# Optimization experiments

Hardware: AMD Instinct MI355X
Metric: run time of the kernel (lower is better)

## Reference

```python
import jax, jax.numpy as jnp
from jax import lax
import numpy as np

HID = 150     # FFNN hidden dim
EMB = 300     # GloVe dim (input_dim)
LSTM = 200    # lstm_dim -> state_dim = 400
T = 768       # tokens in doc
VOCAB = 50000


def _ffnn(x, W1, b1, W2, b2, W3, b3):
    h = jax.nn.relu(x @ W1.T + b1)
    h = jax.nn.relu(h @ W2.T + b2)
    return h @ W3.T + b3


def _lstm_dir(x, Wih, Whh, b):
    H = Whh.shape[1]
    def step(carry, xt):
        h, c = carry
        z = xt @ Wih.T + h @ Whh.T + b
        i, f, g, o = jnp.split(z, 4, axis=-1)
        c = jax.nn.sigmoid(f) * c + jax.nn.sigmoid(i) * jnp.tanh(g)
        h = jax.nn.sigmoid(o) * jnp.tanh(c)
        return (h, c), h
    init = (jnp.zeros((H,), x.dtype), jnp.zeros((H,), x.dtype))
    _, hs = lax.scan(step, init, x)
    return hs


def setup_inputs():
    key = jax.random.key(0)
    ks = iter(jax.random.split(key, 40))
    def w(shape, s=0.05):
        return jax.random.normal(next(ks), shape, jnp.float32) * s
    state = 2 * LSTM
    span = 2 * state + EMB + 1   # 1101
    pair = 3 * span              # 3303
    z = lambda n: jnp.zeros((n,), jnp.float32)
    return {
        'tokens': jax.random.randint(next(ks), (T,), 0, VOCAB),
        'emb': w((VOCAB, EMB), 0.3),
        'Wih_f': w((4 * LSTM, EMB)), 'Whh_f': w((4 * LSTM, LSTM)), 'b_f': z(4 * LSTM),
        'Wih_b': w((4 * LSTM, EMB)), 'Whh_b': w((4 * LSTM, LSTM)), 'b_b': z(4 * LSTM),
        'aW1': w((HID, state)), 'ab1': z(HID), 'aW2': w((HID, HID)), 'ab2': z(HID), 'aW3': w((1, HID)), 'ab3': z(1),
        'sW1': w((HID, span)), 'sb1': z(HID), 'sW2': w((HID, HID)), 'sb2': z(HID), 'sW3': w((1, HID)), 'sb3': z(1),
        'pW1': w((HID, pair)), 'pb1': z(HID), 'pW2': w((HID, HID)), 'pb2': z(HID), 'pW3': w((1, HID)), 'pb3': z(1),
    }


def reference(tokens, emb, Wih_f, Whh_f, b_f, Wih_b, Whh_b, b_b,
              aW1, ab1, aW2, ab2, aW3, ab3,
              sW1, sb1, sW2, sb2, sW3, sb3,
              pW1, pb1, pW2, pb2, pW3, pb3):
    Tn = tokens.shape[0]
    x = emb[tokens]  # (T, 300) frozen GloVe embeds
    h = jnp.concatenate([_lstm_dir(x, Wih_f, Whh_f, b_f),
                         _lstm_dir(x[::-1], Wih_b, Whh_b, b_b)[::-1]], axis=-1)  # (T, 400)
    # dropout omitted (eval mode / identity)
    attn_logits = _ffnn(h, aW1, ab1, aW2, ab2, aW3, ab3)[:, 0]  # per-token attn score (T,)
    gs, i1s, i2s = [], [], []
    for n in range(1, 11):  # span widths 1..10
        starts = jnp.arange(Tn - n + 1)
        idx = starts[:, None] + jnp.arange(n)[None, :]           # (S_n, n)
        wgt = jax.nn.softmax(attn_logits[idx], axis=-1)          # per-span softmax over LSTM-state scores
        pooled = jnp.einsum('sn,snd->sd', wgt, x[idx])           # attention pools raw embeds (as original)
        g = jnp.concatenate([h[starts], h[starts + n - 1], pooled,
                             jnp.full((Tn - n + 1, 1), float(n), jnp.float32)], axis=-1)
        gs.append(g); i1s.append(starts); i2s.append(starts + n - 1)
    g = jnp.concatenate(gs, 0)                                    # (S, 1101)
    i1 = jnp.concatenate(i1s, 0); i2 = jnp.concatenate(i2s, 0)
    S = g.shape[0]
    sm = _ffnn(g, sW1, sb1, sW2, sb2, sW3, sb3)[:, 0]             # span scores (S,)
    order = jnp.argsort(-sm)                                      # stable desc sort, as Python sorted(reverse=True)
    i1o, i2o = i1[order], i2[order]
    # greedy overlap filter: keep span if fully taken OR both endpoints free; mark taken only when kept
    def body(k, carry):
        taken, keep = carry
        a, b = i1o[k], i2o[k]
        offs = jnp.clip(a + jnp.arange(10), 0, Tn - 1)
        valid = (a + jnp.arange(10)) <= b
        all_taken = jnp.all(jnp.where(valid, taken[offs], True))
        ok = all_taken | (~taken[a] & ~taken[b])
        keep = keep.at[k].set(ok)
        taken = taken.at[offs].max(valid & ok)
        return (taken, keep)
    _, keep = lax.fori_loop(0, S, body, (jnp.zeros((Tn,), bool), jnp.zeros((S,), bool)))
    K = int(round(Tn * 0.4))
    rank = jnp.cumsum(keep.astype(jnp.int32))
    pos = jnp.where(keep & (rank <= K), rank - 1, S)
    sel = jnp.argsort(pos)[:K]            # first K kept spans, score order (>=T width-1 spans always kept)
    sel = sel[jnp.argsort(i1o[sel])]      # stable sort by span start
    g_f = g[order][sel]; sm_f = sm[order][sel]
    i1_f = i1o[sel]; i2_f = i2o[sel]
    ii, jj = np.tril_indices(K, -1)       # row-major == nested (i, j<i) loop order
    pairs = jnp.concatenate([g_f[ii], g_f[jj], g_f[ii] * g_f[jj]], axis=-1)  # (P, 3303)
    sa = _ffnn(pairs, pW1, pb1, pW2, pb2, pW3, pb3)[:, 0]
    # sij[i, j] = sm_i + sm_j + sa_ij for j < i; diag/upper = 0 (the epsilon antecedent)
    sij = jnp.zeros((K, K), jnp.float32).at[ii, jj].set(sm_f[ii] + sm_f[jj] + sa)
    return sij, i1_f, i2_f
```

## Files before the change

### kernel.cpp

```cpp
#include <hip/hip_runtime.h>
#include <math.h>
#include <float.h>

#define TN      768
#define EMBD    300
#define XPAD    304
#define LSTMD   200
#define G4      800
#define STATE   400
#define HIDD    150
#define NPADC   160
#define SPAND   1101
#define KP      1120
#define NSPANS  7635
#define NSEL    307
#define SORTN   8192

typedef unsigned long long ull;

#define OFF_X       0u
#define OFF_ZXF     233472u
#define OFF_ZXB     847872u
#define OFF_H       1462272u
#define OFF_ATTN    1769472u
#define OFF_I1      1770496u
#define OFF_I2      1778176u
#define OFF_SM      1785856u
#define OFF_SELK    1793536u
#define OFF_SELSPAN 1794048u
#define OFF_SMF     1794560u
#define OFF_A       1795072u
#define OFF_B       1844224u
#define OFF_WTF     1893376u
#define OFF_WTB     2133376u
#define OFF_AW1T    2373376u
#define OFF_AW2T    2437376u
#define OFF_SW1T    2461376u
#define OFF_SW2T    2640576u
#define OFF_PW1AT   2664576u
#define OFF_PW1BT   2843776u
#define OFF_PW1CT   3022976u
#define OFF_PW2T    3202176u
#define OFF_G       3226176u

#define REP50(M) M(0) M(1) M(2) M(3) M(4) M(5) M(6) M(7) M(8) M(9) \
 M(10) M(11) M(12) M(13) M(14) M(15) M(16) M(17) M(18) M(19) \
 M(20) M(21) M(22) M(23) M(24) M(25) M(26) M(27) M(28) M(29) \
 M(30) M(31) M(32) M(33) M(34) M(35) M(36) M(37) M(38) M(39) \
 M(40) M(41) M(42) M(43) M(44) M(45) M(46) M(47) M(48) M(49)

__device__ __forceinline__ float sigf(float x) { return 1.f / (1.f + __expf(-x)); }
__device__ __forceinline__ float tanhf_(float x) {
    x = fminf(15.f, fmaxf(-15.f, x));
    float e = __expf(2.f * x);
    return (e - 1.f) / (e + 1.f);
}

__global__ void k_gather(const int* __restrict__ tokens, const float* __restrict__ emb,
                         float* __restrict__ x) {
    int t = blockIdx.x;
    int tok = tokens[t];
    for (int d = threadIdx.x; d < XPAD; d += 256)
        x[t * XPAD + d] = (d < EMBD) ? emb[(size_t)tok * EMBD + d] : 0.f;
}

__global__ void k_transpose(const float* __restrict__ src, float* __restrict__ dst,
                            int N, int K, int srcStride, int colOff, int Npad) {
    int k = blockIdx.x;
    int n = blockIdx.y * 256 + threadIdx.x;
    if (n >= Npad) return;
    float v = 0.f;
    if (k < K && n < N) v = src[(size_t)n * srcStride + colOff + k];
    dst[(size_t)k * Npad + n] = v;
}

__global__ void k_zx(const float* __restrict__ x, const float* __restrict__ WTf,
                     const float* __restrict__ WTb, const float* __restrict__ bf,
                     const float* __restrict__ bb, float* __restrict__ zxf,
                     float* __restrict__ zxb) {
    __shared__ float xl[8 * XPAD];
    int tid = threadIdx.x;
    int bm = blockIdx.x, dir = blockIdx.y;
    for (int l = tid; l < 8 * XPAD; l += 256) xl[l] = x[(size_t)(bm * 8) * XPAD + l];
    __syncthreads();
    const float* WT = dir ? WTb : WTf;
    const float* bv = dir ? bb : bf;
    float* zx = dir ? zxb : zxf;
    for (int jj = 0; jj < 4; ++jj) {
        int n = tid + 256 * jj;
        if (n >= G4) break;
        float acc[8] = {0, 0, 0, 0, 0, 0, 0, 0};
        for (int k = 0; k < EMBD; ++k) {
            float wv = WT[(size_t)k * G4 + n];
#pragma unroll
            for (int r = 0; r < 8; ++r) acc[r] = fmaf(xl[r * XPAD + k], wv, acc[r]);
        }
        float bias = bv[n];
#pragma unroll
        for (int r = 0; r < 8; ++r) {
            int row = bm * 8 + r;
            int trow = dir ? (TN - 1 - row) : row;
            zx[(size_t)trow * G4 + n] = acc[r] + bias;
        }
    }
}

__global__ __launch_bounds__(256, 1) void k_lstm_mb8(const float* __restrict__ zxf,
                                                     const float* __restrict__ zxb,
                                                     const float* __restrict__ Whh_f,
                                                     const float* __restrict__ Whh_b,
                                                     float* __restrict__ hcat,
                                                     ull* __restrict__ hqL2,
                                                     ull* __restrict__ hqL3) {
    int blk = blockIdx.x;
    int lane8 = blk & 7;
    if (lane8 >= 2) return;
    int dir = lane8, b = blk >> 3;
    int tid = threadIdx.x;

    const float* zx = dir ? zxb : zxf;
    const float* Whh = dir ? Whh_b : Whh_f;
    ull* hq2d = hqL2 + (size_t)dir * TN * 256;
    ull* hq3d = hqL3 + (size_t)dir * TN * 256;
    __shared__ __align__(16) float hprev[LSTMD];
    __shared__ float zl[200];
    bool active = tid < 200;
    int q = tid / 50, u = tid % 50;
    int gr_row = q * 200 + b * 50 + u;
    int grs = active ? gr_row : 0;
    const float4* wr = (const float4*)(Whh + (size_t)grs * LSTMD);
#define WDECL(i) float4 w##i = wr[i];
    REP50(WDECL)
#undef WDECL
    float c = 0.f;
    for (int l = tid; l < LSTMD; l += 256) hprev[l] = 0.f;
    int remote_idx = (tid < b * 50) ? tid : tid + 50;
    int use_fast = 4;
    __syncthreads();
    float zpre = zx[grs];
    for (int t = 0; t < TN; ++t) {
        float acc = zpre;
        const float4* h4 = (const float4*)hprev;
#define WFMA(i) { float4 hv = h4[i]; \
        acc = fmaf(w##i.x, hv.x, acc); acc = fmaf(w##i.y, hv.y, acc); \
        acc = fmaf(w##i.z, hv.z, acc); acc = fmaf(w##i.w, hv.w, acc); }
        REP50(WFMA)
#undef WFMA
        if (active) zl[tid] = acc;
        __syncthreads();
        int trow = dir ? (TN - 1 - t) : t;
        if (tid < 50) {
            float zi = zl[tid], zf = zl[50 + tid], zg = zl[100 + tid], zo = zl[150 + tid];
            c = sigf(zf) * c + sigf(zi) * tanhf_(zg);
            float h = sigf(zo) * tanhf_(c);
            hcat[(size_t)trow * STATE + dir * LSTMD + b * 50 + tid] = h;
            hprev[b * 50 + tid] = h;
            if (t + 1 < TN) {
                ull pk = (ull)__float_as_uint(h) | ((ull)(unsigned)(t + 1) << 32);
                size_t slot = (size_t)t * 256 + b * 50 + tid;
                (void)__hip_atomic_exchange(&hq2d[slot], pk, __ATOMIC_RELAXED,
                                            __HIP_MEMORY_SCOPE_WORKGROUP);
                __hip_atomic_store(&hq3d[slot], pk, __ATOMIC_RELAXED,
                                   __HIP_MEMORY_SCOPE_AGENT);
            }
        }
        if (t + 1 < TN) {
            zpre = zx[(size_t)(t + 1) * G4 + grs];
            if (tid < 150) {
                size_t slot = (size_t)t * 256 + remote_idx;
                ull v = 0;
                bool got = false;
                if (use_fast > 0) {
                    for (int it = 0; it < 8; ++it) {
                        ull probe = ~0ull;
                        __hip_atomic_compare_exchange_strong(
                            &hq2d[slot], &probe, ~0ull, __ATOMIC_RELAXED,
                            __ATOMIC_RELAXED, __HIP_MEMORY_SCOPE_WORKGROUP);
                        if ((unsigned)(probe >> 32) == (unsigned)(t + 1)) {
                            v = probe; got = true; break;
                        }
                    }
                    use_fast = got ? 4 : (use_fast - 1);
                }
                if (!got) {
                    do {
                        v = __hip_atomic_load(&hq3d[slot], __ATOMIC_RELAXED,
                                              __HIP_MEMORY_SCOPE_AGENT);
                    } while ((unsigned)(v >> 32) != (unsigned)(t + 1));
                }
                hprev[remote_idx] = __uint_as_float((unsigned)v);
            }
            __syncthreads();
        }
    }
}

__global__ void k_attn(const float* __restrict__ hcat, const float* __restrict__ aW1T,
                       const float* __restrict__ ab1, const float* __restrict__ aW2T,
                       const float* __restrict__ ab2, const float* __restrict__ aW3,
                       const float* __restrict__ ab3, float* __restrict__ attn) {
    __shared__ float hrow[STATE];
    __shared__ float l1[NPADC];
    __shared__ float l2[NPADC];
    __shared__ float red[256];
    int t = blockIdx.x, tid = threadIdx.x;
    for (int d = tid; d < STATE; d += 256) hrow[d] = hcat[(size_t)t * STATE + d];
    __syncthreads();
    if (tid < HIDD) {
        float acc = ab1[tid];
        for (int k = 0; k < STATE; ++k) acc = fmaf(hrow[k], aW1T[(size_t)k * NPADC + tid], acc);
        l1[tid] = fmaxf(acc, 0.f);
    }
    __syncthreads();
    if (tid < HIDD) {
        float acc = ab2[tid];
        for (int k = 0; k < HIDD; ++k) acc = fmaf(l1[k], aW2T[(size_t)k * NPADC + tid], acc);
        l2[tid] = fmaxf(acc, 0.f);
    }
    __syncthreads();
    float partial = (tid < HIDD) ? l2[tid] * aW3[tid] : 0.f;
    red[tid] = partial;
    __syncthreads();
    for (int s = 128; s > 0; s >>= 1) {
        if (tid < s) red[tid] += red[tid + s];
        __syncthreads();
    }
    if (tid == 0) attn[t] = red[0] + ab3[0];
}

__global__ void k_spans(const float* __restrict__ attn, const float* __restrict__ hcat,
                        const float* __restrict__ x, float* __restrict__ g,
                        int* __restrict__ i1s, int* __restrict__ i2s) {
    int s = blockIdx.x;
    int n = 1, base = 0;
    while (s >= base + (TN - n + 1)) { base += TN - n + 1; n++; }
    int a = s - base, b = a + n - 1;
    int lane = threadIdx.x;
    float e[10];
    float mx = -FLT_MAX;
#pragma unroll
    for (int k = 0; k < 10; ++k)
        if (k < n) { e[k] = attn[a + k]; mx = fmaxf(mx, e[k]); }
    float ssum = 0.f;
#pragma unroll
    for (int k = 0; k < 10; ++k)
        if (k < n) { e[k] = __expf(e[k] - mx); ssum += e[k]; }
    float w[10];
#pragma unroll
    for (int k = 0; k < 10; ++k) w[k] = (k < n) ? e[k] / ssum : 0.f;

    float* grow = g + (size_t)s * KP;
    for (int d = lane; d < STATE; d += 64) grow[d] = hcat[(size_t)a * STATE + d];
    for (int d = lane; d < STATE; d += 64) grow[STATE + d] = hcat[(size_t)b * STATE + d];
    for (int d = lane; d < EMBD; d += 64) {
        float p = 0.f;
#pragma unroll
        for (int k = 0; k < 10; ++k)
            if (k < n) p = fmaf(w[k], x[(size_t)(a + k) * XPAD + d], p);
        grow[2 * STATE + d] = p;
    }
    if (lane == 0) { grow[1100] = (float)n; i1s[s] = a; i2s[s] = b; }
    for (int d = SPAND + lane; d < KP; d += 64) grow[d] = 0.f;
}

__global__ void k_sm(const float* __restrict__ g, const float* __restrict__ sW1T,
                     const float* __restrict__ sb1, const float* __restrict__ sW2T,
                     const float* __restrict__ sb2, const float* __restrict__ sW3,
                     const float* __restrict__ sb3, float* __restrict__ smo) {
    __shared__ float As[32 * 33];
    __shared__ float Bs[32 * NPADC];
    __shared__ float L1[32 * 161];
    int tid = threadIdx.x;
    int tx = tid & 31, ty = tid >> 5;
    int row0 = blockIdx.x * 32;
    float acc[4][5] = {};
    for (int kb = 0; kb < KP; kb += 32) {
        for (int l = tid; l < 32 * 32; l += 256) {
            int r = l >> 5, cc = l & 31;
            int gr = row0 + r;
            As[r * 33 + cc] = (gr < NSPANS) ? g[(size_t)gr * KP + kb + cc] : 0.f;
        }
        for (int l = tid; l < 32 * NPADC; l += 256) {
            int r = l / NPADC, cc = l - NPADC * r;
            Bs[l] = sW1T[(size_t)(kb + r) * NPADC + cc];
        }
        __syncthreads();
        for (int kk = 0; kk < 32; ++kk) {
            float bv[5];
#pragma unroll
            for (int jn = 0; jn < 5; ++jn) bv[jn] = Bs[kk * NPADC + tx + 32 * jn];
#pragma unroll
            for (int i4 = 0; i4 < 4; ++i4) {
                float av = As[(ty * 4 + i4) * 33 + kk];
#pragma unroll
                for (int jn = 0; jn < 5; ++jn) acc[i4][jn] = fmaf(av, bv[jn], acc[i4][jn]);
            }
        }
        __syncthreads();
    }
#pragma unroll
    for (int i4 = 0; i4 < 4; ++i4)
#pragma unroll
        for (int jn = 0; jn < 5; ++jn) {
            int nn = tx + 32 * jn;
            float v = acc[i4][jn] + (nn < HIDD ? sb1[nn] : 0.f);
            L1[(ty * 4 + i4) * 161 + nn] = fmaxf(v, 0.f);
        }
    __syncthreads();
    float acc2[4][5] = {};
    for (int kk = 0; kk < HIDD; ++kk) {
        float bv[5];
#pragma unroll
        for (int jn = 0; jn < 5; ++jn) bv[jn] = sW2T[(size_t)kk * NPADC + tx + 32 * jn];
#pragma unroll
        for (int i4 = 0; i4 < 4; ++i4) {
            float av = L1[(ty * 4 + i4) * 161 + kk];
#pragma unroll
            for (int jn = 0; jn < 5; ++jn) acc2[i4][jn] = fmaf(av, bv[jn], acc2[i4][jn]);
        }
    }
    float part[4];
#pragma unroll
    for (int i4 = 0; i4 < 4; ++i4) {
        float p = 0.f;
#pragma unroll
        for (int jn = 0; jn < 5; ++jn) {
            int nn = tx + 32 * jn;
            float v = acc2[i4][jn] + (nn < HIDD ? sb2[nn] : 0.f);
            v = fmaxf(v, 0.f);
            p = fmaf(v, (nn < HIDD ? sW3[nn] : 0.f), p);
        }
        part[i4] = p;
    }
    for (int s = 16; s > 0; s >>= 1)
#pragma unroll
        for (int i4 = 0; i4 < 4; ++i4) part[i4] += __shfl_xor(part[i4], s, 32);
    if (tx == 0)
#pragma unroll
        for (int i4 = 0; i4 < 4; ++i4) {
            int gr = row0 + ty * 4 + i4;
            if (gr < NSPANS) smo[gr] = part[i4] + sb3[0];
        }
}

__global__ __launch_bounds__(1024) void k_sortsel(const float* __restrict__ sm,
                                                  const int* __restrict__ i1s,
                                                  const int* __restrict__ i2s,
                                                  int* __restrict__ selk,
                                                  int* __restrict__ selspan,
                                                  float* __restrict__ smf,
                                                  float* __restrict__ out) {
    __shared__ float ks[SORTN];
    __shared__ unsigned short id16[SORTN];
    __shared__ int ka2[512];
    __shared__ int va2[512];
    int tid = threadIdx.x;
    for (int i = tid; i < SORTN; i += 1024) {
        ks[i] = (i < NSPANS) ? sm[i] : -FLT_MAX;
        id16[i] = (unsigned short)i;
    }
    __syncthreads();
    for (int size = 2; size <= SORTN; size <<= 1) {
        for (int stride = size >> 1; stride > 0; stride >>= 1) {
            for (int t = tid; t < SORTN / 2; t += 1024) {
                int i = ((t & ~(stride - 1)) << 1) | (t & (stride - 1));
                int j = i + stride;
                float ki = ks[i], kj = ks[j];
                unsigned short ai = id16[i], aj = id16[j];
                bool less_ji = (kj > ki) || (kj == ki && aj < ai);
                bool asc = ((i & size) == 0);
                if (less_ji == asc) {
                    ks[i] = kj; ks[j] = ki;
                    id16[i] = aj; id16[j] = ai;
                }
            }
            __syncthreads();
        }
    }
    unsigned* abu = reinterpret_cast<unsigned*>(ks);
    for (int k = tid; k < NSPANS; k += 1024) {
        int sid = id16[k];
        abu[k] = (unsigned)i1s[sid] | ((unsigned)i2s[sid] << 16);
    }
    __syncthreads();
    if (tid < 64) {
        int l = tid;
        unsigned tk = 0;
        int cnt = 0;
        for (int k = 0; k < NSPANS && cnt < NSEL; ++k) {
            unsigned ab = abu[k];
            int a = (int)(ab & 0xFFFFu), b = (int)(ab >> 16);
            int lo = a - (l << 5), hi = b - (l << 5);
            lo = lo < 0 ? 0 : lo;
            hi = hi > 31 ? 31 : hi;
            unsigned m = 0;
            if (hi >= lo) {
                unsigned upper = (hi == 31) ? 0xFFFFFFFFu : ((1u << (hi + 1)) - 1u);
                m = upper & ~((1u << lo) - 1u);
            }
            bool cov = ((tk & m) == m);
            bool all_taken = __all((int)cov);
            int la = a >> 5, lb = b >> 5;
            unsigned long long bal_a = __ballot((int)((l == la) && ((tk >> (a & 31)) & 1u)));
            unsigned long long bal_b = __ballot((int)((l == lb) && ((tk >> (b & 31)) & 1u)));
            bool ok = all_taken || (bal_a == 0ull && bal_b == 0ull);
            if (ok) {
                tk |= m;
                if (l == 0) selk[cnt] = k;
                cnt++;
            }
        }
    }
    __syncthreads();
    if (tid < 512) {
        int r = tid;
        int key = 0x7FFFFFFF;
        if (r < NSEL) {
            int k = selk[r];
            int a = (int)(abu[k] & 0xFFFFu);
            key = (a << 9) | r;
        }
        ka2[r] = key;
        va2[r] = r;
    }
    __syncthreads();
    for (int size = 2; size <= 512; size <<= 1) {
        for (int stride = size >> 1; stride > 0; stride >>= 1) {
            if (tid < 256) {
                int t = tid;
                int i = ((t & ~(stride - 1)) << 1) | (t & (stride - 1));
                int j = i + stride;
                int ki = ka2[i], kj = ka2[j];
                bool asc = ((i & size) == 0);
                if ((kj < ki) == asc) {
                    ka2[i] = kj; ka2[j] = ki;
                    int vi = va2[i]; va2[i] = va2[j]; va2[j] = vi;
                }
            }
            __syncthreads();
        }
    }
    if (tid < NSEL) {
        int r = va2[tid];
        int k = selk[r];
        int sid = id16[k];
        unsigned ab = abu[k];
        selspan[tid] = sid;
        smf[tid] = sm[sid];
        out[NSEL * NSEL + tid] = (float)(ab & 0xFFFFu);
        out[NSEL * NSEL + NSEL + tid] = (float)(ab >> 16);
    }
}

__global__ void k_AB(const float* __restrict__ g, const int* __restrict__ selspan,
                     const float* __restrict__ pW1aT, const float* __restrict__ pW1bT,
                     const float* __restrict__ pb1, float* __restrict__ Aw,
                     float* __restrict__ Bw) {
    __shared__ float grow[KP];
    int r = blockIdx.x, which = blockIdx.y;
    int sid = selspan[r];
    int tid = threadIdx.x;
    for (int d = tid; d < KP; d += 256) grow[d] = g[(size_t)sid * KP + d];
    __syncthreads();
    if (tid < NPADC) {
        const float* WT = which ? pW1bT : pW1aT;
        float acc = 0.f;
        for (int k = 0; k < KP; ++k) acc = fmaf(grow[k], WT[(size_t)k * NPADC + tid], acc);
        if (which == 0) acc += (tid < HIDD ? pb1[tid] : 0.f);
        (which ? Bw : Aw)[(size_t)r * NPADC + tid] = acc;
    }
}

__global__ void k_pairs(const float* __restrict__ g, const int* __restrict__ selspan,
                        const float* __restrict__ smf, const float* __restrict__ Aw,
                        const float* __restrict__ Bw, const float* __restrict__ pW1cT,
                        const float* __restrict__ pW2T, const float* __restrict__ pb2,
                        const float* __restrict__ pW3, const float* __restrict__ pb3,
                        float* __restrict__ out) {
    int i = blockIdx.x;
    int j0 = blockIdx.y * 32;
    if (j0 >= i) return;
    __shared__ float Gj[32 * 33];
    __shared__ float Gi[32];
    __shared__ float Bs[32 * NPADC];
    __shared__ float L1s[32 * 161];
    int tid = threadIdx.x;
    int tx = tid & 31, ty = tid >> 5;
    int sidi = selspan[i];
    float acc[4][5] = {};
    for (int kb = 0; kb < KP; kb += 32) {
        for (int l = tid; l < 32 * 32; l += 256) {
            int r = l >> 5, cc = l & 31;
            int j = j0 + r;
            int sidj = selspan[j < i ? j : 0];
            Gj[r * 33 + cc] = (j < i) ? g[(size_t)sidj * KP + kb + cc] : 0.f;
        }
        if (tid < 32) Gi[tid] = g[(size_t)sidi * KP + kb + tid];
        for (int l = tid; l < 32 * NPADC; l += 256) {
            int r = l / NPADC, cc = l - NPADC * r;
            Bs[l] = pW1cT[(size_t)(kb + r) * NPADC + cc];
        }
        __syncthreads();
        for (int kk = 0; kk < 32; ++kk) {
            float gik = Gi[kk];
            float bv[5];
#pragma unroll
            for (int jn = 0; jn < 5; ++jn) bv[jn] = Bs[kk * NPADC + tx + 32 * jn];
#pragma unroll
            for (int i4 = 0; i4 < 4; ++i4) {
                float av = Gj[(ty * 4 + i4) * 33 + kk] * gik;
#pragma unroll
                for (int jn = 0; jn < 5; ++jn) acc[i4][jn] = fmaf(av, bv[jn], acc[i4][jn]);
            }
        }
        __syncthreads();
    }
#pragma unroll
    for (int i4 = 0; i4 < 4; ++i4) {
        int m = ty * 4 + i4;
        int j = j0 + m;
        int jsafe = j < i ? j : 0;
#pragma unroll
        for (int jn = 0; jn < 5; ++jn) {
            int nn = tx + 32 * jn;
            float v = acc[i4][jn] + Aw[(size_t)i * NPADC + nn] + Bw[(size_t)jsafe * NPADC + nn];
            L1s[m * 161 + nn] = fmaxf(v, 0.f);
        }
    }
    __syncthreads();
    float acc2[4][5] = {};
    for (int kk = 0; kk < HIDD; ++kk) {
        float bv[5];
#pragma unroll
        for (int jn = 0; jn < 5; ++jn) bv[jn] = pW2T[(size_t)kk * NPADC + tx + 32 * jn];
#pragma unroll
        for (int i4 = 0; i4 < 4; ++i4) {
            float av = L1s[(ty * 4 + i4) * 161 + kk];
#pragma unroll
            for (int jn = 0; jn < 5; ++jn) acc2[i4][jn] = fmaf(av, bv[jn], acc2[i4][jn]);
        }
    }
    float part[4];
#pragma unroll
    for (int i4 = 0; i4 < 4; ++i4) {
        float p = 0.f;
#pragma unroll
        for (int jn = 0; jn < 5; ++jn) {
            int nn = tx + 32 * jn;
            float v = acc2[i4][jn] + (nn < HIDD ? pb2[nn] : 0.f);
            v = fmaxf(v, 0.f);
            p = fmaf(v, (nn < HIDD ? pW3[nn] : 0.f), p);
        }
        part[i4] = p;
    }
    for (int s = 16; s > 0; s >>= 1)
#pragma unroll
        for (int i4 = 0; i4 < 4; ++i4) part[i4] += __shfl_xor(part[i4], s, 32);
    if (tx == 0)
#pragma unroll
        for (int i4 = 0; i4 < 4; ++i4) {
            int j = j0 + ty * 4 + i4;
            if (j < i) out[(size_t)i * NSEL + j] = smf[i] + smf[j] + part[i4] + pb3[0];
        }
}

extern "C" void kernel_launch(void* const* d_in, const int* in_sizes, int n_in,
                              void* d_out, int out_size, void* d_ws, size_t ws_size,
                              hipStream_t stream) {
    (void)in_sizes; (void)n_in; (void)ws_size;
    const int* tokens  = (const int*)d_in[0];
    const float* emb   = (const float*)d_in[1];
    const float* Wih_f = (const float*)d_in[2];
    const float* Whh_f = (const float*)d_in[3];
    const float* b_f   = (const float*)d_in[4];
    const float* Wih_b = (const float*)d_in[5];
    const float* Whh_b = (const float*)d_in[6];
    const float* b_b   = (const float*)d_in[7];
    const float* aW1 = (const float*)d_in[8];  const float* ab1 = (const float*)d_in[9];
    const float* aW2 = (const float*)d_in[10]; const float* ab2 = (const float*)d_in[11];
    const float* aW3 = (const float*)d_in[12]; const float* ab3 = (const float*)d_in[13];
    const float* sW1 = (const float*)d_in[14]; const float* sb1 = (const float*)d_in[15];
    const float* sW2 = (const float*)d_in[16]; const float* sb2 = (const float*)d_in[17];
    const float* sW3 = (const float*)d_in[18]; const float* sb3 = (const float*)d_in[19];
    const float* pW1 = (const float*)d_in[20]; const float* pb1 = (const float*)d_in[21];
    const float* pW2 = (const float*)d_in[22]; const float* pb2 = (const float*)d_in[23];
    const float* pW3 = (const float*)d_in[24]; const float* pb3 = (const float*)d_in[25];
    float* W = (float*)d_ws;
    float* out = (float*)d_out;
    ull* hqL2 = (ull*)(W + OFF_G);
    ull* hqL3 = hqL2 + (size_t)2 * TN * 256;

    hipMemsetAsync(d_out, 0, (size_t)out_size * sizeof(float), stream);
    hipMemsetAsync(hqL2, 0, (size_t)4 * TN * 256 * sizeof(ull), stream);

    k_gather<<<TN, 256, 0, stream>>>(tokens, emb, W + OFF_X);

    k_transpose<<<dim3(300, 4), 256, 0, stream>>>(Wih_f, W + OFF_WTF, 800, 300, 300, 0, 800);
    k_transpose<<<dim3(300, 4), 256, 0, stream>>>(Wih_b, W + OFF_WTB, 800, 300, 300, 0, 800);
    k_transpose<<<dim3(400, 1), 256, 0, stream>>>(aW1, W + OFF_AW1T, 150, 400, 400, 0, NPADC);
    k_transpose<<<dim3(150, 1), 256, 0, stream>>>(aW2, W + OFF_AW2T, 150, 150, 150, 0, NPADC);
    k_transpose<<<dim3(KP, 1), 256, 0, stream>>>(sW1, W + OFF_SW1T, 150, SPAND, SPAND, 0, NPADC);
    k_transpose<<<dim3(150, 1), 256, 0, stream>>>(sW2, W + OFF_SW2T, 150, 150, 150, 0, NPADC);
    k_transpose<<<dim3(KP, 1), 256, 0, stream>>>(pW1, W + OFF_PW1AT, 150, SPAND, 3303, 0, NPADC);
    k_transpose<<<dim3(KP, 1), 256, 0, stream>>>(pW1, W + OFF_PW1BT, 150, SPAND, 3303, 1101, NPADC);
    k_transpose<<<dim3(KP, 1), 256, 0, stream>>>(pW1, W + OFF_PW1CT, 150, SPAND, 3303, 2202, NPADC);
    k_transpose<<<dim3(150, 1), 256, 0, stream>>>(pW2, W + OFF_PW2T, 150, 150, 150, 0, NPADC);

    k_zx<<<dim3(96, 2), 256, 0, stream>>>(W + OFF_X, W + OFF_WTF, W + OFF_WTB, b_f, b_b,
                                          W + OFF_ZXF, W + OFF_ZXB);
    k_lstm_mb8<<<32, 256, 0, stream>>>(W + OFF_ZXF, W + OFF_ZXB, Whh_f, Whh_b, W + OFF_H,
                                       hqL2, hqL3);
    k_attn<<<TN, 256, 0, stream>>>(W + OFF_H, W + OFF_AW1T, ab1, W + OFF_AW2T, ab2, aW3, ab3,
                                   W + OFF_ATTN);
    k_spans<<<NSPANS, 64, 0, stream>>>(W + OFF_ATTN, W + OFF_H, W + OFF_X, W + OFF_G,
                                       (int*)(W + OFF_I1), (int*)(W + OFF_I2));
    k_sm<<<(NSPANS + 31) / 32, 256, 0, stream>>>(W + OFF_G, W + OFF_SW1T, sb1, W + OFF_SW2T, sb2,
                                                 sW3, sb3, W + OFF_SM);
    k_sortsel<<<1, 1024, 0, stream>>>(W + OFF_SM, (int*)(W + OFF_I1), (int*)(W + OFF_I2),
                                      (int*)(W + OFF_SELK), (int*)(W + OFF_SELSPAN),
                                      W + OFF_SMF, out);
    k_AB<<<dim3(NSEL, 2), 256, 0, stream>>>(W + OFF_G, (int*)(W + OFF_SELSPAN), W + OFF_PW1AT,
                                            W + OFF_PW1BT, pb1, W + OFF_A, W + OFF_B);
    k_pairs<<<dim3(NSEL, 10), 256, 0, stream>>>(W + OFF_G, (int*)(W + OFF_SELSPAN), W + OFF_SMF,
                                                W + OFF_A, W + OFF_B, W + OFF_PW1CT, W + OFF_PW2T,
                                                pb2, pW3, pb3, out);
}
```

Before: 2.597 ms.

## Use bf16 MFMA for pair-scoring FFNN layers instead of fp32 FMA

Rewrites the pair-scoring kernel so both the 1101-wide elementwise-product layer and the 150x150 second layer run on bf16 MFMA 16x16x32 instructions. The pair weights are converted once to padded bf16 row-major buffers, replacing the fp32 transposes. The gi*gj product is formed in fp32, rounded to bf16 and staged in LDS with larger K chunks of 224. This cuts the fp32 FMA work in the dominant pair stage, at the cost of bf16 precision in the pair scores.

```diff
diff --git a/kernel.cpp b/kernel.cpp
--- a/kernel.cpp
+++ b/kernel.cpp
@@ -1,4 +1,5 @@
 #include <hip/hip_runtime.h>
+#include <hip/hip_bf16.h>
 #include <math.h>
 #include <float.h>
 
@@ -17,6 +18,8 @@
 #define SORTN   8192
 
 typedef unsigned long long ull;
+typedef __attribute__((ext_vector_type(8))) short bf16x8;
+typedef __attribute__((ext_vector_type(4))) float mf32x4;
 
 #define OFF_X       0u
 #define OFF_ZXF     233472u
@@ -42,6 +45,8 @@
 #define OFF_PW1CT   3022976u
 #define OFF_PW2T    3202176u
 #define OFF_G       3226176u
+#define OFF_PW1CB   11777376u
+#define OFF_PW2B    11866976u
 
 #define REP50(M) M(0) M(1) M(2) M(3) M(4) M(5) M(6) M(7) M(8) M(9) \
  M(10) M(11) M(12) M(13) M(14) M(15) M(16) M(17) M(18) M(19) \
@@ -54,6 +59,10 @@
     x = fminf(15.f, fmaxf(-15.f, x));
     float e = __expf(2.f * x);
     return (e - 1.f) / (e + 1.f);
+}
+__device__ __forceinline__ unsigned short f2bf(float v) {
+    __hip_bfloat16 h = __float2bfloat16(v);
+    return *(unsigned short*)&h;
 }
 
 __global__ void k_gather(const int* __restrict__ tokens, const float* __restrict__ emb,
@@ -72,6 +81,20 @@
     float v = 0.f;
     if (k < K && n < N) v = src[(size_t)n * srcStride + colOff + k];
     dst[(size_t)k * Npad + n] = v;
+}
+
+__global__ void k_bf16w(const float* __restrict__ pW1, const float* __restrict__ pW2,
+                        unsigned short* __restrict__ pw1cb,
+                        unsigned short* __restrict__ pw2b) {
+    int r = blockIdx.x;
+    for (int k = threadIdx.x; k < 1120; k += 256) {
+        float v = (r < 150 && k < 1101) ? pW1[(size_t)r * 3303 + 2202 + k] : 0.f;
+        pw1cb[(size_t)r * 1120 + k] = f2bf(v);
+    }
+    for (int k = threadIdx.x; k < 160; k += 256) {
+        float v = (r < 150 && k < 150) ? pW2[(size_t)r * 150 + k] : 0.f;
+        pw2b[(size_t)r * 160 + k] = f2bf(v);
+    }
 }
 
 __global__ void k_zx(const float* __restrict__ x, const float* __restrict__ WTf,
@@ -471,97 +494,156 @@
     }
 }
 
-__global__ void k_pairs(const float* __restrict__ g, const int* __restrict__ selspan,
-                        const float* __restrict__ smf, const float* __restrict__ Aw,
-                        const float* __restrict__ Bw, const float* __restrict__ pW1cT,
-                        const float* __restrict__ pW2T, const float* __restrict__ pb2,
-                        const float* __restrict__ pW3, const float* __restrict__ pb3,
-                        float* __restrict__ out) {
+__global__ __launch_bounds__(256, 1) void k_pairs_mfma(
+    const float* __restrict__ g, const int* __restrict__ selspan,
+    const float* __restrict__ smf, const float* __restrict__ Aw,
+    const float* __restrict__ Bw, const unsigned short* __restrict__ pw1cb,
+    const unsigned short* __restrict__ pw2b, const float* __restrict__ pb2,
+    const float* __restrict__ pW3, const float* __restrict__ pb3,
+    float* __restrict__ out) {
     int i = blockIdx.x;
     int j0 = blockIdx.y * 32;
     if (j0 >= i) return;
-    __shared__ float Gj[32 * 33];
-    __shared__ float Gi[32];
-    __shared__ float Bs[32 * NPADC];
-    __shared__ float L1s[32 * 161];
+    __shared__ __align__(16) unsigned short Abuf[32][232];
+    __shared__ __align__(16) unsigned short Btb[160][232];
+    __shared__ __align__(16) unsigned short L1b[32][168];
+    __shared__ float BwS[32][160];
+    __shared__ float AwS[160];
+    __shared__ float GiS[224];
+    __shared__ float pb2S[160], pw3S[160];
+    __shared__ float parts[4][32];
     int tid = threadIdx.x;
-    int tx = tid & 31, ty = tid >> 5;
+    int lane = tid & 63, wv = tid >> 6;
+    int l15 = lane & 15, lg = lane >> 4;
     int sidi = selspan[i];
-    float acc[4][5] = {};
-    for (int kb = 0; kb < KP; kb += 32) {
-        for (int l = tid; l < 32 * 32; l += 256) {
-            int r = l >> 5, cc = l & 31;
+
+    if (tid < 160) {
+        AwS[tid] = Aw[(size_t)i * NPADC + tid];
+        pb2S[tid] = (tid < HIDD) ? pb2[tid] : 0.f;
+        pw3S[tid] = (tid < HIDD) ? pW3[tid] : 0.f;
+    }
+    for (int idx = tid; idx < 32 * 160; idx += 256) {
+        int r = idx / 160; int c = idx - r * 160;
+        int j = j0 + r;
+        BwS[r][c] = Bw[(size_t)(j < i ? j : 0) * NPADC + c];
+    }
+    mf32x4 acc[2][3];
+#pragma unroll
+    for (int m = 0; m < 2; ++m)
+#pragma unroll
+        for (int t = 0; t < 3; ++t) acc[m][t] = (mf32x4){0.f, 0.f, 0.f, 0.f};
+
+    for (int kc = 0; kc < KP; kc += 224) {
+        if (tid < 56)
+            *(float4*)&GiS[tid * 4] = *(const float4*)&g[(size_t)sidi * KP + kc + tid * 4];
+        for (int idx = tid; idx < 160 * 28; idx += 256) {
+            int r = idx / 28, s = idx - r * 28;
+            uint4 v = *(const uint4*)(pw1cb + (size_t)r * 1120 + kc + s * 8);
+            *(uint4*)&Btb[r][s * 8] = v;
+        }
+        __syncthreads();
+        for (int idx = tid; idx < 32 * 56; idx += 256) {
+            int r = idx / 56, s = idx - r * 56;
             int j = j0 + r;
-            int sidj = selspan[j < i ? j : 0];
-            Gj[r * 33 + cc] = (j < i) ? g[(size_t)sidj * KP + kb + cc] : 0.f;
-        }
-        if (tid < 32) Gi[tid] = g[(size_t)sidi * KP + kb + tid];
-        for (int l = tid; l < 32 * NPADC; l += 256) {
-            int r = l / NPADC, cc = l - NPADC * r;
-            Bs[l] = pW1cT[(size_t)(kb + r) * NPADC + cc];
+            float4 gj = {0.f, 0.f, 0.f, 0.f};
+            if (j < i) gj = *(const float4*)&g[(size_t)selspan[j] * KP + kc + s * 4];
+            float4 gi = *(const float4*)&GiS[s * 4];
+            ushort4 u;
+            u.x = f2bf(gj.x * gi.x); u.y = f2bf(gj.y * gi.y);
+            u.z = f2bf(gj.z * gi.z); u.w = f2bf(gj.w * gi.w);
+            *(ushort4*)&Abuf[r][s * 4] = u;
         }
         __syncthreads();
-        for (int kk = 0; kk < 32; ++kk) {
-            float gik = Gi[kk];
-            float bv[5];
-#pragma unroll
-            for (int jn = 0; jn < 5; ++jn) bv[jn] = Bs[kk * NPADC + tx + 32 * jn];
-#pragma unroll
-            for (int i4 = 0; i4 < 4; ++i4) {
-                float av = Gj[(ty * 4 + i4) * 33 + kk] * gik;
-#pragma unroll
-                for (int jn = 0; jn < 5; ++jn) acc[i4][jn] = fmaf(av, bv[jn], acc[i4][jn]);
+#pragma unroll
+        for (int kk = 0; kk < 7; ++kk) {
+            int ko = kk * 32 + lg * 8;
+            bf16x8 a0 = *(const bf16x8*)&Abuf[l15][ko];
+            bf16x8 a1 = *(const bf16x8*)&Abuf[16 + l15][ko];
+#pragma unroll
+            for (int t = 0; t < 3; ++t) {
+                int n = wv + 4 * t;
+                if (n < 10) {
+                    bf16x8 bb = *(const bf16x8*)&Btb[n * 16 + l15][ko];
+                    acc[0][t] = __builtin_amdgcn_mfma_f32_16x16x32_bf16(a0, bb, acc[0][t], 0, 0, 0);
+                    acc[1][t] = __builtin_amdgcn_mfma_f32_16x16x32_bf16(a1, bb, acc[1][t], 0, 0, 0);
+                }
             }
         }
         __syncthreads();
     }
 #pragma unroll
-    for (int i4 = 0; i4 < 4; ++i4) {
-        int m = ty * 4 + i4;
-        int j = j0 + m;
-        int jsafe = j < i ? j : 0;
-#pragma unroll
-        for (int jn = 0; jn < 5; ++jn) {
-            int nn = tx + 32 * jn;
-            float v = acc[i4][jn] + Aw[(size_t)i * NPADC + nn] + Bw[(size_t)jsafe * NPADC + nn];
-            L1s[m * 161 + nn] = fmaxf(v, 0.f);
-        }
-    }
-    __syncthreads();
-    float acc2[4][5] = {};
-    for (int kk = 0; kk < HIDD; ++kk) {
-        float bv[5];
-#pragma unroll
-        for (int jn = 0; jn < 5; ++jn) bv[jn] = pW2T[(size_t)kk * NPADC + tx + 32 * jn];
-#pragma unroll
-        for (int i4 = 0; i4 < 4; ++i4) {
-            float av = L1s[(ty * 4 + i4) * 161 + kk];
-#pragma unroll
-            for (int jn = 0; jn < 5; ++jn) acc2[i4][jn] = fmaf(av, bv[jn], acc2[i4][jn]);
-        }
-    }
-    float part[4];
-#pragma unroll
-    for (int i4 = 0; i4 < 4; ++i4) {
-        float p = 0.f;
-#pragma unroll
-        for (int jn = 0; jn < 5; ++jn) {
-            int nn = tx + 32 * jn;
-            float v = acc2[i4][jn] + (nn < HIDD ? pb2[nn] : 0.f);
-            v = fmaxf(v, 0.f);
-            p = fmaf(v, (nn < HIDD ? pW3[nn] : 0.f), p);
-        }
-        part[i4] = p;
-    }
-    for (int s = 16; s > 0; s >>= 1)
-#pragma unroll
-        for (int i4 = 0; i4 < 4; ++i4) part[i4] += __shfl_xor(part[i4], s, 32);
-    if (tx == 0)
-#pragma unroll
-        for (int i4 = 0; i4 < 4; ++i4) {
-            int j = j0 + ty * 4 + i4;
-            if (j < i) out[(size_t)i * NSEL + j] = smf[i] + smf[j] + part[i4] + pb3[0];
-        }
+    for (int m = 0; m < 2; ++m)
+#pragma unroll
+        for (int t = 0; t < 3; ++t) {
+            int n = wv + 4 * t;
+            if (n < 10) {
+#pragma unroll
+                for (int q = 0; q < 4; ++q) {
+                    int row = m * 16 + lg * 4 + q;
+                    int col = n * 16 + l15;
+                    float v = acc[m][t][q] + AwS[col] + BwS[row][col];
+                    L1b[row][col] = f2bf(fmaxf(v, 0.f));
+                }
+            }
+        }
+    for (int idx = tid; idx < 160 * 20; idx += 256) {
+        int r = idx / 20, s = idx - r * 20;
+        *(uint4*)&Btb[r][s * 8] = *(const uint4*)(pw2b + (size_t)r * 160 + s * 8);
+    }
+    __syncthreads();
+    mf32x4 acc2[2][3];
+#pragma unroll
+    for (int m = 0; m < 2; ++m)
+#pragma unroll
+        for (int t = 0; t < 3; ++t) acc2[m][t] = (mf32x4){0.f, 0.f, 0.f, 0.f};
+#pragma unroll
+    for (int kk = 0; kk < 5; ++kk) {
+        int ko = kk * 32 + lg * 8;
+        bf16x8 a0 = *(const bf16x8*)&L1b[l15][ko];
+        bf16x8 a1 = *(const bf16x8*)&L1b[16 + l15][ko];
+#pragma unroll
+        for (int t = 0; t < 3; ++t) {
+            int n = wv + 4 * t;
+            if (n < 10) {
+                bf16x8 bb = *(const bf16x8*)&Btb[n * 16 + l15][ko];
+                acc2[0][t] = __builtin_amdgcn_mfma_f32_16x16x32_bf16(a0, bb, acc2[0][t], 0, 0, 0);
+                acc2[1][t] = __builtin_amdgcn_mfma_f32_16x16x32_bf16(a1, bb, acc2[1][t], 0, 0, 0);
+            }
+        }
+    }
+    float s[2][4] = {};
+#pragma unroll
+    for (int m = 0; m < 2; ++m)
+#pragma unroll
+        for (int t = 0; t < 3; ++t) {
+            int n = wv + 4 * t;
+            if (n < 10) {
+#pragma unroll
+                for (int q = 0; q < 4; ++q) {
+                    int col = n * 16 + l15;
+                    float v = fmaxf(acc2[m][t][q] + pb2S[col], 0.f);
+                    s[m][q] = fmaf(v, pw3S[col], s[m][q]);
+                }
+            }
+        }
+#pragma unroll
+    for (int off = 1; off < 16; off <<= 1)
+#pragma unroll
+        for (int m = 0; m < 2; ++m)
+#pragma unroll
+            for (int q = 0; q < 4; ++q) s[m][q] += __shfl_xor(s[m][q], off);
+    if (l15 == 0) {
+#pragma unroll
+        for (int m = 0; m < 2; ++m)
+#pragma unroll
+            for (int q = 0; q < 4; ++q) parts[wv][m * 16 + lg * 4 + q] = s[m][q];
+    }
+    __syncthreads();
+    if (tid < 32) {
+        float sa = parts[0][tid] + parts[1][tid] + parts[2][tid] + parts[3][tid];
+        int j = j0 + tid;
+        if (j < i) out[(size_t)i * NSEL + j] = smf[i] + smf[j] + sa + pb3[0];
+    }
 }
 
 extern "C" void kernel_launch(void* const* d_in, const int* in_sizes, int n_in,
@@ -589,6 +671,8 @@
     float* out = (float*)d_out;
     ull* hqL2 = (ull*)(W + OFF_G);
     ull* hqL3 = hqL2 + (size_t)2 * TN * 256;
+    unsigned short* pw1cb = (unsigned short*)(W + OFF_PW1CB);
+    unsigned short* pw2b  = (unsigned short*)(W + OFF_PW2B);
 
     hipMemsetAsync(d_out, 0, (size_t)out_size * sizeof(float), stream);
     hipMemsetAsync(hqL2, 0, (size_t)4 * TN * 256 * sizeof(ull), stream);
@@ -603,8 +687,7 @@
     k_transpose<<<dim3(150, 1), 256, 0, stream>>>(sW2, W + OFF_SW2T, 150, 150, 150, 0, NPADC);
     k_transpose<<<dim3(KP, 1), 256, 0, stream>>>(pW1, W + OFF_PW1AT, 150, SPAND, 3303, 0, NPADC);
     k_transpose<<<dim3(KP, 1), 256, 0, stream>>>(pW1, W + OFF_PW1BT, 150, SPAND, 3303, 1101, NPADC);
-    k_transpose<<<dim3(KP, 1), 256, 0, stream>>>(pW1, W + OFF_PW1CT, 150, SPAND, 3303, 2202, NPADC);
-    k_transpose<<<dim3(150, 1), 256, 0, stream>>>(pW2, W + OFF_PW2T, 150, 150, 150, 0, NPADC);
+    k_bf16w<<<160, 256, 0, stream>>>(pW1, pW2, pw1cb, pw2b);
 
     k_zx<<<dim3(96, 2), 256, 0, stream>>>(W + OFF_X, W + OFF_WTF, W + OFF_WTB, b_f, b_b,
                                           W + OFF_ZXF, W + OFF_ZXB);
@@ -621,7 +704,7 @@
                                       W + OFF_SMF, out);
     k_AB<<<dim3(NSEL, 2), 256, 0, stream>>>(W + OFF_G, (int*)(W + OFF_SELSPAN), W + OFF_PW1AT,
                                             W + OFF_PW1BT, pb1, W + OFF_A, W + OFF_B);
-    k_pairs<<<dim3(NSEL, 10), 256, 0, stream>>>(W + OFF_G, (int*)(W + OFF_SELSPAN), W + OFF_SMF,
-                                                W + OFF_A, W + OFF_B, W + OFF_PW1CT, W + OFF_PW2T,
-                                                pb2, pW3, pb3, out);
-}
+    k_pairs_mfma<<<dim3(NSEL, 10), 256, 0, stream>>>(W + OFF_G, (int*)(W + OFF_SELSPAN),
+                                                     W + OFF_SMF, W + OFF_A, W + OFF_B,
+                                                     pw1cb, pw2b, pb2, pW3, pb3, out);
+}
```

Measured after the change: 2.218 ms. -14.6%, faster.
